# Performance work log

Hardware: AMD Instinct MI355X
Metric: run time of the kernel (lower is better)

## Reference

```python
import jax, jax.numpy as jnp
import numpy as np

B, S, D = 16384, 50, 64        # batch, max_seq_len, model_dim
POS = 4                        # pos_emb_dim
CTX = D + POS                  # context_dim fed to W_q (target emb + pos emb) = 68
H1, H2 = 80, 40                # attention_hidden_units


def setup_inputs() -> dict:
    key = jax.random.key(0)
    ks = jax.random.split(key, 12)
    inv = lambda n: 1.0 / np.sqrt(n)
    return {
        "target_emb": jax.random.normal(ks[0], (B, D), jnp.float32),
        "sequence_emb": jax.random.normal(ks[1], (B, S, D), jnp.float32),
        "mask": jax.random.randint(ks[2], (B, S), 0, 2, jnp.int32),
        "pos_emb": jnp.zeros((S, POS), jnp.float32),
        "Wq": jax.random.uniform(ks[3], (CTX, D), jnp.float32, -inv(CTX), inv(CTX)),
        "bq": jax.random.uniform(ks[4], (D,), jnp.float32, -inv(CTX), inv(CTX)),
        "alpha": jnp.full((D,), 0.1, jnp.float32),  # PReLU per-channel slope
        "W1": jax.random.uniform(ks[5], (4 * D, H1), jnp.float32, -inv(4 * D), inv(4 * D)),
        "b1": jax.random.uniform(ks[6], (H1,), jnp.float32, -inv(4 * D), inv(4 * D)),
        "W2": jax.random.uniform(ks[7], (H1, H2), jnp.float32, -inv(H1), inv(H1)),
        "b2": jax.random.uniform(ks[8], (H2,), jnp.float32, -inv(H1), inv(H1)),
        "W3": jax.random.uniform(ks[9], (H2, 1), jnp.float32, -inv(H2), inv(H2)),
        "b3": jax.random.uniform(ks[10], (1,), jnp.float32, -inv(H2), inv(H2)),
    }


def reference(target_emb, sequence_emb, mask, pos_emb, Wq, bq, alpha,
              W1, b1, W2, b2, W3, b3):
    seq_len = sequence_emb.shape[1]
    # context_emb = target broadcast over seq, concat positional embedding -> [B, S, D+POS]
    ctx = jnp.concatenate(
        [jnp.broadcast_to(target_emb[:, None, :], (target_emb.shape[0], seq_len, target_emb.shape[1])),
         jnp.broadcast_to(pos_emb[None, :, :], (target_emb.shape[0], seq_len, pos_emb.shape[1]))],
        axis=-1)
    # W_q: Linear + PReLU (per-channel)
    q = jnp.einsum('bsc,cd->bsd', ctx, Wq) + bq
    query = jnp.where(q >= 0, q, alpha * q)                       # [B, S, D]
    # concat [q, k, q-k, q*k] -> [B, S, 4D]
    inp = jnp.concatenate([query, sequence_emb, query - sequence_emb, query * sequence_emb], axis=-1)
    # attention MLP: 4D -> 80 -> 40 -> 1, Sigmoid hidden activations
    h = jax.nn.sigmoid(jnp.einsum('bsc,ch->bsh', inp, W1) + b1)
    h = jax.nn.sigmoid(jnp.einsum('bsh,hk->bsk', h, W2) + b2)
    attn_score = (jnp.einsum('bsk,ko->bso', h, W3) + b3)[..., 0]  # [B, S]
    m = mask == 0
    p = jax.nn.softmax(jnp.where(m, -1e9, attn_score), axis=-1)
    attn_out = jnp.einsum('bs,bsd->bd', p, sequence_emb)          # [B, D]
    rel_i2i = jnp.sum(jnp.where(m, 0.0, attn_score), axis=1, keepdims=True)  # [B, 1]
    return attn_out, rel_i2i
```

## Files before the change

kernel.cpp:

```cpp
#include <hip/hip_runtime.h>
#include <stdint.h>

#define BB   16384
#define SS   50
#define DD   64
#define NH1  80
#define NB   16
#define MT   50

#define WS_UVW_SHORTS   (30*64*8)
#define WS_W2F_OFF      WS_UVW_SHORTS
#define WS_W2F_SHORTS   (9*64*8)
#define WS_QP_BYTE_OFF  (2*(WS_UVW_SHORTS+WS_W2F_SHORTS))
#define WS_QP_FLOATS    (SS*DD)

typedef short bf16x8 __attribute__((ext_vector_type(8)));
typedef float f32x4  __attribute__((ext_vector_type(4)));
typedef int   i32x4  __attribute__((ext_vector_type(4)));

__device__ inline short f2bf(float x) {
    union { float f; uint32_t u; } v; v.f = x;
    uint32_t r = (v.u + 0x7FFFu + ((v.u >> 16) & 1u)) >> 16;
    return (short)r;
}
__device__ inline float fexp(float x)  { return __builtin_amdgcn_exp2f(x * 1.44269504f); }
__device__ inline float fsig(float x)  { return __builtin_amdgcn_rcpf(1.f + fexp(-x)); }

__global__ __launch_bounds__(256) void i2i_prep(
    const float* __restrict__ pos, const float* __restrict__ Wq,
    const float* __restrict__ bq,  const float* __restrict__ W1,
    const float* __restrict__ W2,  short* __restrict__ ws_s,
    float* __restrict__ qp)
{
    int gid = blockIdx.x * 256 + threadIdx.x;
    if (gid < 1920) {
        int frag = gid >> 6, lane = gid & 63;
        int t = frag / 6, ks = frag % 6;
        int i16 = lane & 15, g = lane >> 4;
        int h = 16*t + i16;
        int kbase = 32*ks + 8*g;
        short tmp[8];
        #pragma unroll
        for (int j = 0; j < 8; ++j) {
            int k = kbase + j;
            float v;
            if (k < 64)       v = W1[k*NH1 + h] + W1[(128+k)*NH1 + h];
            else if (k < 128) v = W1[k*NH1 + h] - W1[(k+64)*NH1 + h];
            else              v = W1[(k+64)*NH1 + h];
            tmp[j] = f2bf(v);
        }
        *(bf16x8*)&ws_s[gid*8] = *(bf16x8*)tmp;
    } else if (gid < 1920 + 576) {
        int idx = gid - 1920;
        int frag = idx >> 6, lane = idx & 63;
        int t = frag / 3, ks = frag % 3;
        int i16 = lane & 15, g = lane >> 4;
        int c = 16*t + i16;
        int kbase = 32*ks + 8*g;
        short tmp[8];
        #pragma unroll
        for (int j = 0; j < 8; ++j) {
            int k = kbase + j;
            float v = (c < 40 && k < 80) ? W2[k*40 + c] : 0.f;
            tmp[j] = f2bf(v);
        }
        *(bf16x8*)&ws_s[WS_W2F_OFF + idx*8] = *(bf16x8*)tmp;
    } else if (gid < 1920 + 576 + WS_QP_FLOATS) {
        int idx = gid - 1920 - 576;
        int s = idx >> 6, d = idx & 63;
        float acc = bq[d];
        #pragma unroll
        for (int p = 0; p < 4; ++p) acc += pos[s*4 + p] * Wq[(64+p)*64 + d];
        qp[idx] = acc;
    }
}

__global__ __launch_bounds__(256, 3) void i2i_kernel(
    const float* __restrict__ target, const float* __restrict__ seq,
    const int*   __restrict__ mask,   const float* __restrict__ Wq,
    const float* __restrict__ alpha,  const float* __restrict__ b1,
    const float* __restrict__ b2,     const float* __restrict__ W3,
    const float* __restrict__ b3,     const short* __restrict__ ws_s,
    const float* __restrict__ qp,     float* __restrict__ out)
{
    __shared__ short uvw[30*512];
    __shared__ float qtLDS[16][68];
    __shared__ float scores[16][52];
    __shared__ short h1buf[4][16][104];

    const int tid  = threadIdx.x;
    const int wg   = blockIdx.x;
    const int b0   = wg * NB;
    const int lane = tid & 63;
    const int wv   = tid >> 6;

    #pragma unroll
    for (int o = 0; o < 8; ++o) {
        int idx = tid + o*256;
        if (idx < 1920) ((i32x4*)uvw)[idx] = ((const i32x4*)ws_s)[idx];
    }
    for (int o = tid; o < 4*16*16; o += 256)
        h1buf[o >> 8][(o >> 4) & 15][80 + (o & 15)] = 0;
    {
        int d = tid & 63, l0 = tid >> 6;
        for (int lb = l0; lb < NB; lb += 4) {
            const float* trow = target + (size_t)(b0 + lb) * DD;
            float acc = 0.f;
            #pragma unroll 8
            for (int c = 0; c < DD; ++c) acc += trow[c] * Wq[c*DD + d];
            qtLDS[lb][d] = acc;
        }
    }

    const int i16 = lane & 15;
    const int g   = lane >> 4;
    const int dA  = 8 * g, dB = 32 + 8 * g;

    bf16x8 bw2[3][3];
    #pragma unroll
    for (int t = 0; t < 3; ++t)
        #pragma unroll
        for (int ks = 0; ks < 3; ++ks)
            bw2[t][ks] = *(const bf16x8*)&ws_s[WS_W2F_OFF + ((t*3+ks)*64 + lane)*8];

    float b1v[5], b2v[3], w3v[3];
    #pragma unroll
    for (int t = 0; t < 5; ++t) b1v[t] = b1[i16 + 16*t];
    #pragma unroll
    for (int t = 0; t < 3; ++t) {
        int c = i16 + 16*t;
        b2v[t] = (c < 40) ? b2[c] : 0.f;
        w3v[t] = (c < 40) ? W3[c] : 0.f;
    }
    const float b3v = b3[0];
    __syncthreads();

    #pragma unroll 1
    for (int mt = wv; mt < MT; mt += 4) {
        const int rloc = mt*16 + i16;
        const int lb   = rloc / 50;
        const int s    = rloc - lb*50;
        const int R    = wg*800 + rloc;
        const float* srow = seq + (size_t)R * DD;
        const float* qprow = qp + s*DD;

        bf16x8 a[6];
        #pragma unroll
        for (int c = 0; c < 4; ++c) {
            const int d0 = (c < 2 ? dA : dB) + (c & 1) * 4;
            const int fi = c >> 1;
            f32x4 x  = *(const f32x4*)&qtLDS[lb][d0] + *(const f32x4*)&qprow[d0];
            f32x4 al = *(const f32x4*)&alpha[d0];
            f32x4 sq = *(const f32x4*)&srow[d0];
            #pragma unroll
            for (int j = 0; j < 4; ++j) {
                const int li = (c & 1)*4 + j;
                float xx = x[j];
                float qv = xx >= 0.f ? xx : al[j]*xx;
                float kv = sq[j];
                a[0+fi][li] = f2bf(qv);
                a[2+fi][li] = f2bf(kv);
                a[4+fi][li] = f2bf(qv*kv);
            }
        }

        f32x4 acc1[5];
        #pragma unroll
        for (int t = 0; t < 5; ++t) {
            f32x4 c = {0.f,0.f,0.f,0.f};
            #pragma unroll
            for (int ks = 0; ks < 6; ++ks) {
                bf16x8 bf = *(const bf16x8*)&uvw[(t*6+ks)*512 + lane*8];
                c = __builtin_amdgcn_mfma_f32_16x16x32_bf16(a[ks], bf, c, 0, 0, 0);
            }
            acc1[t] = c;
        }
        #pragma unroll
        for (int t = 0; t < 5; ++t)
            #pragma unroll
            for (int ii = 0; ii < 4; ++ii)
                h1buf[wv][4*g + ii][i16 + 16*t] = f2bf(fsig(acc1[t][ii] + b1v[t]));
        asm volatile("s_waitcnt lgkmcnt(0)" ::: "memory");

        f32x4 acc2[3];
        #pragma unroll
        for (int t = 0; t < 3; ++t) acc2[t] = (f32x4){0.f,0.f,0.f,0.f};
        #pragma unroll
        for (int ks = 0; ks < 3; ++ks) {
            bf16x8 a2 = *(const bf16x8*)&h1buf[wv][i16][32*ks + 8*g];
            #pragma unroll
            for (int t = 0; t < 3; ++t)
                acc2[t] = __builtin_amdgcn_mfma_f32_16x16x32_bf16(a2, bw2[t][ks], acc2[t], 0, 0, 0);
        }
        float sc[4];
        #pragma unroll
        for (int ii = 0; ii < 4; ++ii) {
            float v = 0.f;
            #pragma unroll
            for (int t = 0; t < 3; ++t)
                v += fsig(acc2[t][ii] + b2v[t]) * w3v[t];
            sc[ii] = v;
        }
        #pragma unroll
        for (int off = 1; off < 16; off <<= 1)
            #pragma unroll
            for (int ii = 0; ii < 4; ++ii)
                sc[ii] += __shfl_xor(sc[ii], off, 64);
        if (i16 == 0) {
            #pragma unroll
            for (int ii = 0; ii < 4; ++ii) {
                int row = mt*16 + 4*g + ii;
                int lb2 = row / 50, s2 = row - lb2*50;
                scores[lb2][s2] = sc[ii] + b3v;
            }
        }
    }
    __syncthreads();

    for (int lb = wv*4; lb < wv*4 + 4; ++lb) {
        const int b = b0 + lb;
        float sval = 0.f; int mval = 0;
        if (lane < SS) { sval = scores[lb][lane]; mval = mask[b*SS + lane]; }
        float ms = (lane < SS) ? (mval != 0 ? sval : -1e9f) : -INFINITY;
        float M = ms;
        #pragma unroll
        for (int off = 1; off < 64; off <<= 1) M = fmaxf(M, __shfl_xor(M, off, 64));
        float e = fexp(ms - M);
        float Ssum = e;
        #pragma unroll
        for (int off = 1; off < 64; off <<= 1) Ssum += __shfl_xor(Ssum, off, 64);
        float p = e * __builtin_amdgcn_rcpf(Ssum);
        float rel = (lane < SS && mval != 0) ? sval : 0.f;
        #pragma unroll
        for (int off = 1; off < 64; off <<= 1) rel += __shfl_xor(rel, off, 64);
        if (lane < SS) scores[lb][lane] = p;
        asm volatile("s_waitcnt lgkmcnt(0)" ::: "memory");

        const float* sb = seq + (size_t)b * SS * DD;
        float accd = 0.f;
        #pragma unroll 10
        for (int s = 0; s < SS; ++s)
            accd += scores[lb][s] * sb[s*DD + lane];
        out[(size_t)b * DD + lane] = accd;
        if (lane == 0) out[(size_t)BB * DD + b] = rel;
    }
}

extern "C" void kernel_launch(void* const* d_in, const int* in_sizes, int n_in,
                              void* d_out, int out_size, void* d_ws, size_t ws_size,
                              hipStream_t stream) {
    const float* target = (const float*)d_in[0];
    const float* seq    = (const float*)d_in[1];
    const int*   mask   = (const int*)d_in[2];
    const float* pos    = (const float*)d_in[3];
    const float* Wq     = (const float*)d_in[4];
    const float* bq     = (const float*)d_in[5];
    const float* alpha  = (const float*)d_in[6];
    const float* b1     = (const float*)d_in[8];
    const float* W1     = (const float*)d_in[7];
    const float* W2     = (const float*)d_in[9];
    const float* b2     = (const float*)d_in[10];
    const float* W3     = (const float*)d_in[11];
    const float* b3     = (const float*)d_in[12];
    float* outp = (float*)d_out;

    short* ws_s = (short*)d_ws;
    float* qp   = (float*)((char*)d_ws + WS_QP_BYTE_OFF);

    hipLaunchKernelGGL(i2i_prep, dim3(23), dim3(256), 0, stream,
                       pos, Wq, bq, W1, W2, ws_s, qp);
    hipLaunchKernelGGL(i2i_kernel, dim3(BB / NB), dim3(256), 0, stream,
                       target, seq, mask, Wq, alpha, b1, b2, W3, b3, ws_s, qp, outp);
}
```

Before: 125.5 us.

## Double workgroup size to 32 rows and prefetch next sequence tile into registers

Each workgroup now handles 32 batch rows with 8 waves (512 threads), which amortises the per-block LDS weight load and target projection over more rows. Each wave also software-prefetches the next 16-row sequence tile into registers while it runs the MFMA work on the current tile, to hide global load latency. The cost is more LDS per block, higher register pressure from the prefetch buffers, and half as many blocks. The unseen tail code must handle NB=32 and 8 waves correctly.

```diff
diff --git a/kernel.cpp b/kernel.cpp
--- a/kernel.cpp
+++ b/kernel.cpp
@@ -5,8 +5,9 @@
 #define SS   50
 #define DD   64
 #define NH1  80
-#define NB   16
-#define MT   50
+#define NB   32
+#define MT   100
+#define NWAVE 8
 
 #define WS_UVW_SHORTS   (30*64*8)
 #define WS_W2F_OFF      WS_UVW_SHORTS
@@ -75,7 +76,7 @@
     }
 }
 
-__global__ __launch_bounds__(256, 3) void i2i_kernel(
+__global__ __launch_bounds__(512, 4) void i2i_kernel(
     const float* __restrict__ target, const float* __restrict__ seq,
     const int*   __restrict__ mask,   const float* __restrict__ Wq,
     const float* __restrict__ alpha,  const float* __restrict__ b1,
@@ -84,9 +85,9 @@
     const float* __restrict__ qp,     float* __restrict__ out)
 {
     __shared__ short uvw[30*512];
-    __shared__ float qtLDS[16][68];
-    __shared__ float scores[16][52];
-    __shared__ short h1buf[4][16][104];
+    __shared__ float qtLDS[NB][68];
+    __shared__ float scores[NB][52];
+    __shared__ short h1buf[NWAVE][16][104];
 
     const int tid  = threadIdx.x;
     const int wg   = blockIdx.x;
@@ -95,15 +96,15 @@
     const int wv   = tid >> 6;
 
     #pragma unroll
-    for (int o = 0; o < 8; ++o) {
-        int idx = tid + o*256;
+    for (int o = 0; o < 4; ++o) {
+        int idx = tid + o*512;
         if (idx < 1920) ((i32x4*)uvw)[idx] = ((const i32x4*)ws_s)[idx];
     }
-    for (int o = tid; o < 4*16*16; o += 256)
+    for (int o = tid; o < NWAVE*16*16; o += 512)
         h1buf[o >> 8][(o >> 4) & 15][80 + (o & 15)] = 0;
     {
         int d = tid & 63, l0 = tid >> 6;
-        for (int lb = l0; lb < NB; lb += 4) {
+        for (int lb = l0; lb < NB; lb += NWAVE) {
             const float* trow = target + (size_t)(b0 + lb) * DD;
             float acc = 0.f;
             #pragma unroll 8
@@ -135,13 +136,19 @@
     const float b3v = b3[0];
     __syncthreads();
 
+    f32x4 cur[4];
+    {
+        const float* srow0 = seq + (size_t)(wg*(NB*SS) + wv*16 + i16) * DD;
+        #pragma unroll
+        for (int c = 0; c < 4; ++c)
+            cur[c] = *(const f32x4*)&srow0[(c < 2 ? dA : dB) + (c & 1)*4];
+    }
+
     #pragma unroll 1
-    for (int mt = wv; mt < MT; mt += 4) {
+    for (int mt = wv; mt < MT; mt += NWAVE) {
         const int rloc = mt*16 + i16;
         const int lb   = rloc / 50;
         const int s    = rloc - lb*50;
-        const int R    = wg*800 + rloc;
-        const float* srow = seq + (size_t)R * DD;
         const float* qprow = qp + s*DD;
 
         bf16x8 a[6];
@@ -151,7 +158,7 @@
             const int fi = c >> 1;
             f32x4 x  = *(const f32x4*)&qtLDS[lb][d0] + *(const f32x4*)&qprow[d0];
             f32x4 al = *(const f32x4*)&alpha[d0];
-            f32x4 sq = *(const f32x4*)&srow[d0];
+            f32x4 sq = cur[c];
             #pragma unroll
             for (int j = 0; j < 4; ++j) {
                 const int li = (c & 1)*4 + j;
@@ -162,6 +169,14 @@
                 a[2+fi][li] = f2bf(kv);
                 a[4+fi][li] = f2bf(qv*kv);
             }
+        }
+
+        {
+            const int mtn = (mt + NWAVE < MT) ? mt + NWAVE : mt;
+            const float* srown = seq + (size_t)(wg*(NB*SS) + mtn*16 + i16) * DD;
+            #pragma unroll
+            for (int c = 0; c < 4; ++c)
+                cur[c] = *(const f32x4*)&srown[(c < 2 ? dA : dB) + (c & 1)*4];
         }
 
         f32x4 acc1[5];
@@ -256,8 +271,8 @@
     const float* Wq     = (const float*)d_in[4];
     const float* bq     = (const float*)d_in[5];
     const float* alpha  = (const float*)d_in[6];
+    const float* W1     = (const float*)d_in[7];
     const float* b1     = (const float*)d_in[8];
-    const float* W1     = (const float*)d_in[7];
     const float* W2     = (const float*)d_in[9];
     const float* b2     = (const float*)d_in[10];
     const float* W3     = (const float*)d_in[11];
@@ -269,6 +284,6 @@
 
     hipLaunchKernelGGL(i2i_prep, dim3(23), dim3(256), 0, stream,
                        pos, Wq, bq, W1, W2, ws_s, qp);
-    hipLaunchKernelGGL(i2i_kernel, dim3(BB / NB), dim3(256), 0, stream,
+    hipLaunchKernelGGL(i2i_kernel, dim3(BB / NB), dim3(512), 0, stream,
                        target, seq, mask, Wq, alpha, b1, b2, W3, b3, ws_s, qp, outp);
 }
```

New measurement: 164.8 us. 31.3% more time.
